# Kernel tuning notes

Hardware: AMD Instinct MI355X
Metric: run time of the kernel (lower is better)

Reference implementation:

```python
import jax, jax.numpy as jnp
import numpy as np
import math

D_MODEL, N_LEVELS, N_HEADS, N_POINTS = 256, 4, 8, 4
D_HEAD = D_MODEL // N_HEADS
SPATIAL = np.array([[128, 128], [64, 64], [32, 32], [16, 16]], dtype=np.int32)  # (H_l, W_l)
LEN_IN = int((SPATIAL[:, 0] * SPATIAL[:, 1]).sum())  # 21760
N_BATCH, LEN_Q = 8, 1000


def _offset_bias():
    # torch _reset_parameters grid_init
    thetas = np.arange(N_HEADS, dtype=np.float32) * (2.0 * math.pi / N_HEADS)
    grid = np.stack([np.cos(thetas), np.sin(thetas)], -1)
    grid = grid / np.abs(grid).max(-1, keepdims=True)
    grid = np.tile(grid.reshape(N_HEADS, 1, 1, 2), (1, N_LEVELS, N_POINTS, 1))
    for i in range(N_POINTS):
        grid[:, :, i, :] *= i + 1
    return jnp.asarray(grid.reshape(-1), dtype=jnp.float32)


def setup_inputs() -> dict:
    key = jax.random.key(0)
    ks = jax.random.split(key, 8)
    s = 1.0 / math.sqrt(D_MODEL)
    return {
        "query": jax.random.normal(ks[0], (N_BATCH, LEN_Q, D_MODEL), jnp.float32),
        "reference_points": jax.random.uniform(ks[1], (N_BATCH, LEN_Q, N_LEVELS, 2), jnp.float32),
        "input_flatten": jax.random.normal(ks[2], (N_BATCH, LEN_IN, D_MODEL), jnp.float32),
        "input_spatial_shapes": jnp.asarray(SPATIAL),
        "input_level_start_index": jnp.asarray(np.concatenate([[0], np.cumsum(SPATIAL[:, 0] * SPATIAL[:, 1])[:-1]]).astype(np.int32)),
        # params (W stored as (in, out); y = x @ W + b)
        "W_off": jax.random.normal(ks[3], (D_MODEL, N_HEADS * N_LEVELS * N_POINTS * 2), jnp.float32) * 0.01,
        "b_off": _offset_bias(),
        "W_attn": jax.random.normal(ks[4], (D_MODEL, N_HEADS * N_LEVELS * N_POINTS), jnp.float32) * 0.02,
        "b_attn": jnp.zeros((N_HEADS * N_LEVELS * N_POINTS,), jnp.float32),
        "W_val": jax.random.normal(ks[5], (D_MODEL, D_MODEL), jnp.float32) * s,
        "b_val": jnp.zeros((D_MODEL,), jnp.float32),
        "W_out": jax.random.normal(ks[6], (D_MODEL, D_MODEL), jnp.float32) * s,
        "b_out": jnp.zeros((D_MODEL,), jnp.float32),
    }


def _bilinear_sample(v, x, y, H, W):
    # v: (N, nH, H*W, dH); x, y: (N, nH, Lq, nP) in pixel coords (grid_sample align_corners=False, zeros padding)
    Nb, nH, Lq, nP = x.shape
    x0 = jnp.floor(x); y0 = jnp.floor(y)
    wx1 = x - x0; wy1 = y - y0
    x0i = x0.astype(jnp.int32); y0i = y0.astype(jnp.int32)
    out = jnp.zeros((Nb, nH, Lq, nP, v.shape[-1]), v.dtype)
    for dy, wy in ((0, 1.0 - wy1), (1, wy1)):
        for dx, wx in ((0, 1.0 - wx1), (1, wx1)):
            ix = x0i + dx; iy = y0i + dy
            valid = (ix >= 0) & (ix < W) & (iy >= 0) & (iy < H)
            idx = (jnp.clip(iy, 0, H - 1) * W + jnp.clip(ix, 0, W - 1)).reshape(Nb, nH, Lq * nP, 1)
            g = jnp.take_along_axis(v, idx, axis=2).reshape(Nb, nH, Lq, nP, -1)
            out = out + g * (wy * wx * valid.astype(v.dtype))[..., None]
    return out


def reference(query, reference_points, input_flatten, input_spatial_shapes, input_level_start_index,
              W_off, b_off, W_attn, b_attn, W_val, b_val, W_out, b_out):
    shapes = np.asarray(input_spatial_shapes)          # static metadata
    starts = np.asarray(input_level_start_index)
    Nb, Lq, _ = query.shape

    value = input_flatten @ W_val + b_val              # (N, Lin, C)
    value = value.reshape(Nb, -1, N_HEADS, D_HEAD).transpose(0, 2, 1, 3)  # (N, nH, Lin, dH)

    offsets = (query @ W_off + b_off).reshape(Nb, Lq, N_HEADS, N_LEVELS, N_POINTS, 2)
    attn = jax.nn.softmax((query @ W_attn + b_attn).reshape(Nb, Lq, N_HEADS, N_LEVELS * N_POINTS), axis=-1)
    attn = attn.reshape(Nb, Lq, N_HEADS, N_LEVELS, N_POINTS)

    # normalizer is (W_l, H_l) per level; locations in [0,1]
    normalizer = jnp.asarray(np.stack([shapes[:, 1], shapes[:, 0]], -1), jnp.float32)
    loc = reference_points[:, :, None, :, None, :] + offsets / normalizer[None, None, None, :, None, :]

    out = jnp.zeros((Nb, N_HEADS, Lq, D_HEAD), value.dtype)
    for l in range(N_LEVELS):
        H, W = int(shapes[l, 0]), int(shapes[l, 1])
        s = int(starts[l])
        v_l = value[:, :, s:s + H * W]                             # (N, nH, HW, dH)
        loc_l = loc[:, :, :, l].transpose(0, 2, 1, 3, 4)           # (N, nH, Lq, nP, 2)
        x = loc_l[..., 0] * W - 0.5
        y = loc_l[..., 1] * H - 0.5
        sampled = _bilinear_sample(v_l, x, y, H, W)                # (N, nH, Lq, nP, dH)
        a_l = attn[:, :, :, l].transpose(0, 2, 1, 3)               # (N, nH, Lq, nP)
        out = out + jnp.einsum('nhqpd,nhqp->nhqd', sampled, a_l)

    out = out.transpose(0, 2, 1, 3).reshape(Nb, Lq, D_MODEL)
    return out @ W_out + b_out
```

## Files before the change

### kernel.cpp

```cpp
#include <hip/hip_runtime.h>
#include <hip/hip_bf16.h>

#define D_MODEL 256
#define N_HEADS 8
#define D_HEAD 32
#define N_LEVELS 4
#define N_POINTS 4
#define LEN_IN 21760
#define N_BATCH 8
#define LEN_Q 1000

typedef __attribute__((ext_vector_type(8))) short short8;
typedef __attribute__((ext_vector_type(4))) float f32x4;
typedef __attribute__((ext_vector_type(4))) unsigned int u32x4;

typedef const __attribute__((address_space(1))) void* gp1;
typedef __attribute__((address_space(3))) void* lp3;

__device__ __forceinline__ unsigned short f2bf(float f) {
    unsigned int u = __float_as_uint(f);
    u += 0x7FFFu + ((u >> 16) & 1u);
    return (unsigned short)(u >> 16);
}
__device__ __forceinline__ float bf2f(unsigned short s) {
    return __uint_as_float(((unsigned int)s) << 16);
}
__device__ __forceinline__ unsigned int cvtpk(float lo, float hi) {
    unsigned int r;
    asm("v_cvt_pk_bf16_f32 %0, %1, %2" : "=v"(r) : "v"(lo), "v"(hi));
    return r;
}

__global__ __launch_bounds__(256) void prep_kernel(
    const float* __restrict__ Wv, const float* __restrict__ Wo,
    const float* __restrict__ Wa, const float* __restrict__ Wu,
    const float* __restrict__ boff, const float* __restrict__ battn,
    unsigned short* __restrict__ WtVp, unsigned short* __restrict__ WtC,
    unsigned short* __restrict__ WtO, float* __restrict__ bcat)
{
    int idx = blockIdx.x * 256 + threadIdx.x;
    if (idx < 65536) {
        int j = idx & 7, lane = (idx >> 3) & 63, nf = (idx >> 9) & 15, ks = idx >> 13;
        int col = nf * 16 + (lane & 15);
        int k = ks * 32 + (lane >> 4) * 8 + j;
        WtVp[idx] = f2bf(Wv[k * 256 + col]);
    } else if (idx < 65536 + 98304) {
        int j = idx - 65536;
        int n = j >> 8, k = j & 255;
        float s = (n < 256) ? Wo[k * 256 + n] : Wa[k * 128 + (n - 256)];
        WtC[j] = f2bf(s);
    } else if (idx < 65536 + 98304 + 65536) {
        int j = idx - (65536 + 98304);
        int n = j >> 8, k = j & 255;
        WtO[j] = f2bf(Wu[k * 256 + n]);
    } else if (idx < 65536 + 98304 + 65536 + 384) {
        int j = idx - (65536 + 98304 + 65536);
        bcat[j] = (j < 256) ? boff[j] : battn[j - 256];
    }
}

__global__ __launch_bounds__(256) void gemm_value(
    const float* __restrict__ A,
    const unsigned short* __restrict__ Bp,
    const float* __restrict__ bias,
    unsigned short* __restrict__ C)
{
    __shared__ __align__(16) float lds[2][4096];

    const int tid = threadIdx.x;
    const int wave = tid >> 6, lane = tid & 63;
    const int lhi = lane >> 4, llo = lane & 15;
    const int mBase = blockIdx.x * 64;

    const int srow = tid >> 4;
    const int scg = (tid & 15) ^ (srow & 15);
    const char* Ab = (const char*)(A + (size_t)mBase * 256);

#define STG(bi, kt) { \
    const char* s_ = Ab + (size_t)(kt) * 256 + (size_t)srow * 1024 + scg * 16; \
    char* d_ = (char*)&lds[bi][0] + tid * 16; \
    __builtin_amdgcn_global_load_lds((gp1)(const void*)(s_),         (lp3)(d_),         16, 0, 0); \
    __builtin_amdgcn_global_load_lds((gp1)(const void*)(s_ + 16384), (lp3)(d_ + 4096),  16, 0, 0); \
    __builtin_amdgcn_global_load_lds((gp1)(const void*)(s_ + 32768), (lp3)(d_ + 8192),  16, 0, 0); \
    __builtin_amdgcn_global_load_lds((gp1)(const void*)(s_ + 49152), (lp3)(d_ + 12288), 16, 0, 0); }

    f32x4 acc[4][4];
#pragma unroll
    for (int mf = 0; mf < 4; ++mf)
#pragma unroll
        for (int n = 0; n < 4; ++n)
            acc[mf][n] = (f32x4){0.f, 0.f, 0.f, 0.f};

    STG(0, 0);

#pragma unroll
    for (int kt = 0; kt < 4; ++kt) {
        const int cur = kt & 1;

        short8 b[2][4];
#pragma unroll
        for (int ksi = 0; ksi < 2; ++ksi)
#pragma unroll
            for (int n = 0; n < 4; ++n)
                b[ksi][n] = *reinterpret_cast<const short8*>(
                    Bp + ((size_t)((kt * 2 + ksi) * 16 + wave * 4 + n) * 64 + lane) * 8);

        if (kt < 3) STG(cur ^ 1, kt + 1);

        __builtin_amdgcn_sched_barrier(0);
        if (kt < 3) asm volatile("s_waitcnt vmcnt(12)" ::: "memory");
        else        asm volatile("s_waitcnt vmcnt(8)" ::: "memory");
        __builtin_amdgcn_sched_barrier(0);
        __builtin_amdgcn_s_barrier();
        __builtin_amdgcn_sched_barrier(0);

#pragma unroll
        for (int mf = 0; mf < 4; ++mf) {
            const int row = mf * 16 + llo;
            const char* rbase = (const char*)&lds[cur][0] + row * 256;
#pragma unroll
            for (int ksi = 0; ksi < 2; ++ksi) {
                const int cg0 = ksi * 8 + lhi * 2;
                f32x4 flo = *reinterpret_cast<const f32x4*>(rbase + ((cg0 ^ llo) << 4));
                f32x4 fhi = *reinterpret_cast<const f32x4*>(rbase + (((cg0 + 1) ^ llo) << 4));
                u32x4 pk;
                pk[0] = cvtpk(flo[0], flo[1]);
                pk[1] = cvtpk(flo[2], flo[3]);
                pk[2] = cvtpk(fhi[0], fhi[1]);
                pk[3] = cvtpk(fhi[2], fhi[3]);
                short8 af = __builtin_bit_cast(short8, pk);
#pragma unroll
                for (int n = 0; n < 4; ++n)
                    acc[mf][n] = __builtin_amdgcn_mfma_f32_16x16x32_bf16(
                        af, b[ksi][n], acc[mf][n], 0, 0, 0);
            }
        }

        __builtin_amdgcn_sched_barrier(0);
        __builtin_amdgcn_s_barrier();
        __builtin_amdgcn_sched_barrier(0);
    }
#undef STG

    float bb[4];
#pragma unroll
    for (int n = 0; n < 4; ++n) bb[n] = bias[wave * 64 + n * 16 + llo];
#pragma unroll
    for (int mf = 0; mf < 4; ++mf) {
        const int row0 = mBase + mf * 16 + lhi * 4;
#pragma unroll
        for (int n = 0; n < 4; ++n) {
            const int col = wave * 64 + n * 16 + llo;
            unsigned int u01 = cvtpk(acc[mf][n][0] + bb[n], acc[mf][n][1] + bb[n]);
            unsigned int u23 = cvtpk(acc[mf][n][2] + bb[n], acc[mf][n][3] + bb[n]);
            C[(size_t)(row0 + 0) * 256 + col] = (unsigned short)(u01 & 0xFFFFu);
            C[(size_t)(row0 + 1) * 256 + col] = (unsigned short)(u01 >> 16);
            C[(size_t)(row0 + 2) * 256 + col] = (unsigned short)(u23 & 0xFFFFu);
            C[(size_t)(row0 + 3) * 256 + col] = (unsigned short)(u23 >> 16);
        }
    }
}

template<int NF, bool ABF16, bool OBF16>
__global__ __launch_bounds__(256) void gemm_k256(
    const void* __restrict__ Av, const unsigned short* __restrict__ Wt,
    const float* __restrict__ bias, void* __restrict__ Cv)
{
    const int wave = threadIdx.x >> 6;
    const int lane = threadIdx.x & 63;
    const int lhi = lane >> 4, llo = lane & 15;
    const int mBase = blockIdx.x * 16;
    const int colBase = wave * (NF * 16);
    const int N = NF * 64;

    f32x4 acc[NF];
#pragma unroll
    for (int n = 0; n < NF; ++n)
        acc[n] = (f32x4){0.f, 0.f, 0.f, 0.f};

#pragma unroll
    for (int ks = 0; ks < 8; ++ks) {
        const int kk = ks * 32 + lhi * 8;
        short8 a;
        if (ABF16) {
            a = *reinterpret_cast<const short8*>(
                (const unsigned short*)Av + (size_t)(mBase + llo) * 256 + kk);
        } else {
            const float* ap = (const float*)Av + (size_t)(mBase + llo) * 256 + kk;
            f32x4 f0 = *reinterpret_cast<const f32x4*>(ap);
            f32x4 f1 = *reinterpret_cast<const f32x4*>(ap + 4);
            u32x4 pk;
            pk[0] = cvtpk(f0[0], f0[1]);
            pk[1] = cvtpk(f0[2], f0[3]);
            pk[2] = cvtpk(f1[0], f1[1]);
            pk[3] = cvtpk(f1[2], f1[3]);
            a = __builtin_bit_cast(short8, pk);
        }
        short8 b[NF];
#pragma unroll
        for (int n = 0; n < NF; ++n) {
            const unsigned short* bp =
                Wt + (size_t)(colBase + n * 16 + llo) * 256 + kk;
            b[n] = *reinterpret_cast<const short8*>(bp);
        }
#pragma unroll
        for (int n = 0; n < NF; ++n)
            acc[n] = __builtin_amdgcn_mfma_f32_16x16x32_bf16(
                a, b[n], acc[n], 0, 0, 0);
    }

    const int row0 = mBase + lhi * 4;
#pragma unroll
    for (int n = 0; n < NF; ++n) {
        const int col = colBase + n * 16 + llo;
        const float bb = bias[col];
#pragma unroll
        for (int r = 0; r < 4; ++r) {
            float v = acc[n][r] + bb;
            size_t idx = (size_t)(row0 + r) * N + col;
            if (OBF16) ((unsigned short*)Cv)[idx] = f2bf(v);
            else       ((float*)Cv)[idx] = v;
        }
    }
}

__global__ __launch_bounds__(512) void ms_sample_kernel(
    const unsigned short* __restrict__ value,
    const float* __restrict__ proj,
    const float* __restrict__ refp,
    unsigned short* __restrict__ out_h)
{
    const int bid = blockIdx.x;
    const int b = bid & 7;
    const int q = bid >> 3;
    const int bq = b * LEN_Q + q;

    const int h = threadIdx.x >> 6;
    const int lane = threadIdx.x & 63;
    const int task = lane >> 2;
    const int l = task >> 2;
    const int qd = lane & 3;

    const float* prow = proj + (size_t)bq * 384;

    const int Wl = 128 >> l;
    const int st = (65536 - (65536 >> (l << 1))) / 3;

    const float2 dxy = *reinterpret_cast<const float2*>(prow + h * 32 + 2 * task);
    const float2 rxy = *reinterpret_cast<const float2*>(refp + ((size_t)bq * 4 + l) * 2);

    const float Wlf = (float)Wl;
    const float x = rxy.x * Wlf + dxy.x - 0.5f;
    const float y = rxy.y * Wlf + dxy.y - 0.5f;
    const float x0f = floorf(x), y0f = floorf(y);
    const int x0 = (int)x0f, y0 = (int)y0f;
    const float wx1 = x - x0f, wy1 = y - y0f;
    const float wx0 = 1.f - wx1, wy0 = 1.f - wy1;

    const int x0c = min(max(x0, 0), Wl - 1);
    const int x1c = min(max(x0 + 1, 0), Wl - 1);
    const int y0c = min(max(y0, 0), Wl - 1);
    const int y1c = min(max(y0 + 1, 0), Wl - 1);
    const float fx0 = (x0 >= 0 && x0 < Wl) ? 1.f : 0.f;
    const float fx1 = (x0 + 1 >= 0 && x0 + 1 < Wl) ? 1.f : 0.f;
    const float fy0 = (y0 >= 0 && y0 < Wl) ? 1.f : 0.f;
    const float fy1 = (y0 + 1 >= 0 && y0 + 1 < Wl) ? 1.f : 0.f;

    const int rr0 = st + y0c * Wl, rr1 = st + y1c * Wl;
    const int r00 = rr0 + x0c, r01 = rr0 + x1c;
    const int r10 = rr1 + x0c, r11 = rr1 + x1c;

    const char* vb = (const char*)value + (size_t)b * LEN_IN * 512
                   + h * 64 + qd * 16;
    u32x4 v0 = *reinterpret_cast<const u32x4*>(vb + (size_t)r00 * 512);
    u32x4 v1 = *reinterpret_cast<const u32x4*>(vb + (size_t)r01 * 512);
    u32x4 v2 = *reinterpret_cast<const u32x4*>(vb + (size_t)r10 * 512);
    u32x4 v3 = *reinterpret_cast<const u32x4*>(vb + (size_t)r11 * 512);

    float lg = prow[256 + h * 16 + (lane & 15)];
    float mx = lg;
    mx = fmaxf(mx, __shfl_xor(mx, 1, 16));
    mx = fmaxf(mx, __shfl_xor(mx, 2, 16));
    mx = fmaxf(mx, __shfl_xor(mx, 4, 16));
    mx = fmaxf(mx, __shfl_xor(mx, 8, 16));
    float e = __expf(lg - mx);
    float den = e;
    den += __shfl_xor(den, 1, 16);
    den += __shfl_xor(den, 2, 16);
    den += __shfl_xor(den, 4, 16);
    den += __shfl_xor(den, 8, 16);
    const float wsm = e / den;
    const float ws = __shfl(wsm, task, 16);

    float wgt[4];
    wgt[0] = ws * wy0 * wx0 * fy0 * fx0;
    wgt[1] = ws * wy0 * wx1 * fy0 * fx1;
    wgt[2] = ws * wy1 * wx0 * fy1 * fx0;
    wgt[3] = ws * wy1 * wx1 * fy1 * fx1;

    float acc[8];
#pragma unroll
    for (int j = 0; j < 8; ++j) acc[j] = 0.f;
#pragma unroll
    for (int n = 0; n < 4; ++n) {
        const u32x4 v = (n == 0) ? v0 : (n == 1) ? v1 : (n == 2) ? v2 : v3;
        const float wn = wgt[n];
#pragma unroll
        for (int j = 0; j < 4; ++j) {
            const unsigned int u = v[j];
            acc[2 * j]     += wn * bf2f((unsigned short)(u & 0xFFFFu));
            acc[2 * j + 1] += wn * bf2f((unsigned short)(u >> 16));
        }
    }

#pragma unroll
    for (int j = 0; j < 8; ++j) {
        acc[j] += __shfl_xor(acc[j], 4, 64);
        acc[j] += __shfl_xor(acc[j], 8, 64);
        acc[j] += __shfl_xor(acc[j], 16, 64);
        acc[j] += __shfl_xor(acc[j], 32, 64);
    }

    if (task == 0) {
        u32x4 o;
#pragma unroll
        for (int j = 0; j < 4; ++j)
            o[j] = (unsigned int)f2bf(acc[2 * j]) |
                   ((unsigned int)f2bf(acc[2 * j + 1]) << 16);
        *reinterpret_cast<u32x4*>(
            out_h + (size_t)bq * 256 + h * 32 + qd * 8) = o;
    }
}

extern "C" void kernel_launch(void* const* d_in, const int* in_sizes, int n_in,
                              void* d_out, int out_size, void* d_ws, size_t ws_size,
                              hipStream_t stream)
{
    const float* query  = (const float*)d_in[0];
    const float* refp   = (const float*)d_in[1];
    const float* inpf   = (const float*)d_in[2];
    const float* W_off  = (const float*)d_in[5];
    const float* b_off  = (const float*)d_in[6];
    const float* W_attn = (const float*)d_in[7];
    const float* b_attn = (const float*)d_in[8];
    const float* W_val  = (const float*)d_in[9];
    const float* b_val  = (const float*)d_in[10];
    const float* W_out  = (const float*)d_in[11];
    const float* b_out  = (const float*)d_in[12];

    char* ws = (char*)d_ws;
    unsigned short* value = (unsigned short*)(ws);
    float*          proj  = (float*)(ws + 89128960);
    unsigned short* out_h = (unsigned short*)(ws + 89128960 + 12288000);
    unsigned short* WtVp  = (unsigned short*)(ws + 109608960);
    unsigned short* WtC   = (unsigned short*)(ws + 109740032);
    unsigned short* WtO   = (unsigned short*)(ws + 109936640);
    float*          bcat  = (float*)(ws + 110067712);

    prep_kernel<<<898, 256, 0, stream>>>(W_val, W_off, W_attn, W_out,
                                         b_off, b_attn, WtVp, WtC, WtO, bcat);

    gemm_value<<<(N_BATCH * LEN_IN) / 64, 256, 0, stream>>>(
        inpf, WtVp, b_val, value);

    gemm_k256<6, false, false><<<(N_BATCH * LEN_Q) / 16, 256, 0, stream>>>(
        query, WtC, bcat, (void*)proj);

    ms_sample_kernel<<<N_BATCH * LEN_Q, 512, 0, stream>>>(
        value, proj, refp, out_h);

    gemm_k256<4, true, false><<<(N_BATCH * LEN_Q) / 16, 256, 0, stream>>>(
        out_h, WtO, b_out, d_out);
}
```

Baseline: 128.5 us.

## Retile value GEMM to 128-row blocks with 8 waves and 32-wide K steps

The value projection GEMM now uses 512-thread blocks covering 128 rows, arranged as a 2x4 wave grid. It stages K in 32-float slices across 8 iterations instead of 64-float slices across 4, keeping the same LDS footprint. Each B fragment load is shared by twice as many rows per block, and the per-step wait count drops. The trade is more barriers per block, half as many blocks, and a new swizzle pattern for LDS reads.

```diff
diff --git a/kernel.cpp b/kernel.cpp
--- a/kernel.cpp
+++ b/kernel.cpp
@@ -59,7 +59,7 @@
     }
 }
 
-__global__ __launch_bounds__(256) void gemm_value(
+__global__ __launch_bounds__(512) void gemm_value(
     const float* __restrict__ A,
     const unsigned short* __restrict__ Bp,
     const float* __restrict__ bias,
@@ -69,20 +69,20 @@
 
     const int tid = threadIdx.x;
     const int wave = tid >> 6, lane = tid & 63;
+    const int wr = wave >> 2, wc = wave & 3;
     const int lhi = lane >> 4, llo = lane & 15;
-    const int mBase = blockIdx.x * 64;
-
-    const int srow = tid >> 4;
-    const int scg = (tid & 15) ^ (srow & 15);
+    const int mBase = blockIdx.x * 128;
+
+    const int srow = tid >> 3;
+    const int scg = (tid & 7) ^ (srow & 7);
     const char* Ab = (const char*)(A + (size_t)mBase * 256);
+    const size_t src0 = (size_t)srow * 1024 + (size_t)scg * 16;
 
 #define STG(bi, kt) { \
-    const char* s_ = Ab + (size_t)(kt) * 256 + (size_t)srow * 1024 + scg * 16; \
+    const char* s_ = Ab + (size_t)(kt) * 128 + src0; \
     char* d_ = (char*)&lds[bi][0] + tid * 16; \
-    __builtin_amdgcn_global_load_lds((gp1)(const void*)(s_),         (lp3)(d_),         16, 0, 0); \
-    __builtin_amdgcn_global_load_lds((gp1)(const void*)(s_ + 16384), (lp3)(d_ + 4096),  16, 0, 0); \
-    __builtin_amdgcn_global_load_lds((gp1)(const void*)(s_ + 32768), (lp3)(d_ + 8192),  16, 0, 0); \
-    __builtin_amdgcn_global_load_lds((gp1)(const void*)(s_ + 49152), (lp3)(d_ + 12288), 16, 0, 0); }
+    __builtin_amdgcn_global_load_lds((gp1)(const void*)(s_),         (lp3)(d_),        16, 0, 0); \
+    __builtin_amdgcn_global_load_lds((gp1)(const void*)(s_ + 65536), (lp3)(d_ + 8192), 16, 0, 0); }
 
     f32x4 acc[4][4];
 #pragma unroll
@@ -94,63 +94,58 @@
     STG(0, 0);
 
 #pragma unroll
-    for (int kt = 0; kt < 4; ++kt) {
+    for (int kt = 0; kt < 8; ++kt) {
         const int cur = kt & 1;
 
-        short8 b[2][4];
-#pragma unroll
-        for (int ksi = 0; ksi < 2; ++ksi)
+        short8 b[4];
+#pragma unroll
+        for (int n = 0; n < 4; ++n)
+            b[n] = *reinterpret_cast<const short8*>(
+                Bp + ((size_t)(kt * 16 + wc * 4 + n) * 64 + lane) * 8);
+
+        if (kt < 7) STG(cur ^ 1, kt + 1);
+
+        __builtin_amdgcn_sched_barrier(0);
+        if (kt < 7) asm volatile("s_waitcnt vmcnt(6)" ::: "memory");
+        else        asm volatile("s_waitcnt vmcnt(4)" ::: "memory");
+        __builtin_amdgcn_sched_barrier(0);
+        __builtin_amdgcn_s_barrier();
+        __builtin_amdgcn_sched_barrier(0);
+
+#pragma unroll
+        for (int mf = 0; mf < 4; ++mf) {
+            const int row = wr * 64 + mf * 16 + llo;
+            const char* rbase = (const char*)&lds[cur][0] + row * 128;
+            const int sw = row & 7;
+            f32x4 flo = *reinterpret_cast<const f32x4*>(rbase + (((lhi * 2) ^ sw) << 4));
+            f32x4 fhi = *reinterpret_cast<const f32x4*>(rbase + (((lhi * 2 + 1) ^ sw) << 4));
+            u32x4 pk;
+            pk[0] = cvtpk(flo[0], flo[1]);
+            pk[1] = cvtpk(flo[2], flo[3]);
+            pk[2] = cvtpk(fhi[0], fhi[1]);
+            pk[3] = cvtpk(fhi[2], fhi[3]);
+            short8 af = __builtin_bit_cast(short8, pk);
 #pragma unroll
             for (int n = 0; n < 4; ++n)
-                b[ksi][n] = *reinterpret_cast<const short8*>(
-                    Bp + ((size_t)((kt * 2 + ksi) * 16 + wave * 4 + n) * 64 + lane) * 8);
-
-        if (kt < 3) STG(cur ^ 1, kt + 1);
-
-        __builtin_amdgcn_sched_barrier(0);
-        if (kt < 3) asm volatile("s_waitcnt vmcnt(12)" ::: "memory");
-        else        asm volatile("s_waitcnt vmcnt(8)" ::: "memory");
+                acc[mf][n] = __builtin_amdgcn_mfma_f32_16x16x32_bf16(
+                    af, b[n], acc[mf][n], 0, 0, 0);
+        }
+
         __builtin_amdgcn_sched_barrier(0);
         __builtin_amdgcn_s_barrier();
         __builtin_amdgcn_sched_barrier(0);
-
-#pragma unroll
-        for (int mf = 0; mf < 4; ++mf) {
-            const int row = mf * 16 + llo;
-            const char* rbase = (const char*)&lds[cur][0] + row * 256;
-#pragma unroll
-            for (int ksi = 0; ksi < 2; ++ksi) {
-                const int cg0 = ksi * 8 + lhi * 2;
-                f32x4 flo = *reinterpret_cast<const f32x4*>(rbase + ((cg0 ^ llo) << 4));
-                f32x4 fhi = *reinterpret_cast<const f32x4*>(rbase + (((cg0 + 1) ^ llo) << 4));
-                u32x4 pk;
-                pk[0] = cvtpk(flo[0], flo[1]);
-                pk[1] = cvtpk(flo[2], flo[3]);
-                pk[2] = cvtpk(fhi[0], fhi[1]);
-                pk[3] = cvtpk(fhi[2], fhi[3]);
-                short8 af = __builtin_bit_cast(short8, pk);
-#pragma unroll
-                for (int n = 0; n < 4; ++n)
-                    acc[mf][n] = __builtin_amdgcn_mfma_f32_16x16x32_bf16(
-                        af, b[ksi][n], acc[mf][n], 0, 0, 0);
-            }
-        }
-
-        __builtin_amdgcn_sched_barrier(0);
-        __builtin_amdgcn_s_barrier();
-        __builtin_amdgcn_sched_barrier(0);
     }
 #undef STG
 
     float bb[4];
 #pragma unroll
-    for (int n = 0; n < 4; ++n) bb[n] = bias[wave * 64 + n * 16 + llo];
+    for (int n = 0; n < 4; ++n) bb[n] = bias[wc * 64 + n * 16 + llo];
 #pragma unroll
     for (int mf = 0; mf < 4; ++mf) {
-        const int row0 = mBase + mf * 16 + lhi * 4;
+        const int row0 = mBase + wr * 64 + mf * 16 + lhi * 4;
 #pragma unroll
         for (int n = 0; n < 4; ++n) {
-            const int col = wave * 64 + n * 16 + llo;
+            const int col = wc * 64 + n * 16 + llo;
             unsigned int u01 = cvtpk(acc[mf][n][0] + bb[n], acc[mf][n][1] + bb[n]);
             unsigned int u23 = cvtpk(acc[mf][n][2] + bb[n], acc[mf][n][3] + bb[n]);
             C[(size_t)(row0 + 0) * 256 + col] = (unsigned short)(u01 & 0xFFFFu);
@@ -360,7 +355,7 @@
     prep_kernel<<<898, 256, 0, stream>>>(W_val, W_off, W_attn, W_out,
                                          b_off, b_attn, WtVp, WtC, WtO, bcat);
 
-    gemm_value<<<(N_BATCH * LEN_IN) / 64, 256, 0, stream>>>(
+    gemm_value<<<(N_BATCH * LEN_IN) / 128, 512, 0, stream>>>(
         inpf, WtVp, b_val, value);
 
     gemm_k256<6, false, false><<<(N_BATCH * LEN_Q) / 16, 256, 0, stream>>>(
```

Result: no change. 130.3 us (+1.5%).

## Process four row tiles per block in value GEMM with continuous prefetch pipeline

Applied to the files above, without the earlier changes.

The value projection GEMM now has each block handle 256 rows as four consecutive 64-row tiles. The global-to-LDS double-buffer pipeline runs across tile boundaries, so the next tile's first K-slice is prefetched while the current tile finishes. Each tile's output is written when it completes. The grid shrinks from 2720 to 680 blocks, which cuts launch and prologue overhead but reduces parallelism to fewer blocks per CU and keeps the B fragments reloaded each step.

```diff
diff --git a/kernel.cpp b/kernel.cpp
--- a/kernel.cpp
+++ b/kernel.cpp
@@ -70,14 +70,15 @@
     const int tid = threadIdx.x;
     const int wave = tid >> 6, lane = tid & 63;
     const int lhi = lane >> 4, llo = lane & 15;
-    const int mBase = blockIdx.x * 64;
+    const size_t rowBlk = (size_t)blockIdx.x * 256;
 
     const int srow = tid >> 4;
     const int scg = (tid & 15) ^ (srow & 15);
-    const char* Ab = (const char*)(A + (size_t)mBase * 256);
-
-#define STG(bi, kt) { \
-    const char* s_ = Ab + (size_t)(kt) * 256 + (size_t)srow * 1024 + scg * 16; \
+    const char* Ab = (const char*)(A + rowBlk * 256);
+    const size_t src0 = (size_t)srow * 1024 + (size_t)scg * 16;
+
+#define STG(bi, tile, kt) { \
+    const char* s_ = Ab + (size_t)(tile) * 65536 + (size_t)(kt) * 256 + src0; \
     char* d_ = (char*)&lds[bi][0] + tid * 16; \
     __builtin_amdgcn_global_load_lds((gp1)(const void*)(s_),         (lp3)(d_),         16, 0, 0); \
     __builtin_amdgcn_global_load_lds((gp1)(const void*)(s_ + 16384), (lp3)(d_ + 4096),  16, 0, 0); \
@@ -91,11 +92,15 @@
         for (int n = 0; n < 4; ++n)
             acc[mf][n] = (f32x4){0.f, 0.f, 0.f, 0.f};
 
-    STG(0, 0);
-
-#pragma unroll
-    for (int kt = 0; kt < 4; ++kt) {
-        const int cur = kt & 1;
+    float bb[4];
+#pragma unroll
+    for (int n = 0; n < 4; ++n) bb[n] = bias[wave * 64 + n * 16 + llo];
+
+    STG(0, 0, 0);
+
+#pragma unroll
+    for (int tau = 0; tau < 16; ++tau) {
+        const int tile = tau >> 2, kt = tau & 3, cur = tau & 1;
 
         short8 b[2][4];
 #pragma unroll
@@ -105,11 +110,14 @@
                 b[ksi][n] = *reinterpret_cast<const short8*>(
                     Bp + ((size_t)((kt * 2 + ksi) * 16 + wave * 4 + n) * 64 + lane) * 8);
 
-        if (kt < 3) STG(cur ^ 1, kt + 1);
-
-        __builtin_amdgcn_sched_barrier(0);
-        if (kt < 3) asm volatile("s_waitcnt vmcnt(12)" ::: "memory");
-        else        asm volatile("s_waitcnt vmcnt(8)" ::: "memory");
+        if (tau < 15) {
+            const int nt = tau + 1;
+            STG(nt & 1, nt >> 2, nt & 3);
+        }
+
+        __builtin_amdgcn_sched_barrier(0);
+        if (tau < 15) asm volatile("s_waitcnt vmcnt(12)" ::: "memory");
+        else          asm volatile("s_waitcnt vmcnt(8)" ::: "memory");
         __builtin_amdgcn_sched_barrier(0);
         __builtin_amdgcn_s_barrier();
         __builtin_amdgcn_sched_barrier(0);
@@ -139,26 +147,26 @@
         __builtin_amdgcn_sched_barrier(0);
         __builtin_amdgcn_s_barrier();
         __builtin_amdgcn_sched_barrier(0);
+
+        if (kt == 3) {
+#pragma unroll
+            for (int mf = 0; mf < 4; ++mf) {
+                const int row0 = (int)rowBlk + tile * 64 + mf * 16 + lhi * 4;
+#pragma unroll
+                for (int n = 0; n < 4; ++n) {
+                    const int col = wave * 64 + n * 16 + llo;
+                    unsigned int u01 = cvtpk(acc[mf][n][0] + bb[n], acc[mf][n][1] + bb[n]);
+                    unsigned int u23 = cvtpk(acc[mf][n][2] + bb[n], acc[mf][n][3] + bb[n]);
+                    C[(size_t)(row0 + 0) * 256 + col] = (unsigned short)(u01 & 0xFFFFu);
+                    C[(size_t)(row0 + 1) * 256 + col] = (unsigned short)(u01 >> 16);
+                    C[(size_t)(row0 + 2) * 256 + col] = (unsigned short)(u23 & 0xFFFFu);
+                    C[(size_t)(row0 + 3) * 256 + col] = (unsigned short)(u23 >> 16);
+                    acc[mf][n] = (f32x4){0.f, 0.f, 0.f, 0.f};
+                }
+            }
+        }
     }
 #undef STG
-
-    float bb[4];
-#pragma unroll
-    for (int n = 0; n < 4; ++n) bb[n] = bias[wave * 64 + n * 16 + llo];
-#pragma unroll
-    for (int mf = 0; mf < 4; ++mf) {
-        const int row0 = mBase + mf * 16 + lhi * 4;
-#pragma unroll
-        for (int n = 0; n < 4; ++n) {
-            const int col = wave * 64 + n * 16 + llo;
-            unsigned int u01 = cvtpk(acc[mf][n][0] + bb[n], acc[mf][n][1] + bb[n]);
-            unsigned int u23 = cvtpk(acc[mf][n][2] + bb[n], acc[mf][n][3] + bb[n]);
-            C[(size_t)(row0 + 0) * 256 + col] = (unsigned short)(u01 & 0xFFFFu);
-            C[(size_t)(row0 + 1) * 256 + col] = (unsigned short)(u01 >> 16);
-            C[(size_t)(row0 + 2) * 256 + col] = (unsigned short)(u23 & 0xFFFFu);
-            C[(size_t)(row0 + 3) * 256 + col] = (unsigned short)(u23 >> 16);
-        }
-    }
 }
 
 template<int NF, bool ABF16, bool OBF16>
@@ -360,8 +368,7 @@
     prep_kernel<<<898, 256, 0, stream>>>(W_val, W_off, W_attn, W_out,
                                          b_off, b_attn, WtVp, WtC, WtO, bcat);
 
-    gemm_value<<<(N_BATCH * LEN_IN) / 64, 256, 0, stream>>>(
-        inpf, WtVp, b_val, value);
+    gemm_value<<<680, 256, 0, stream>>>(inpf, WtVp, b_val, value);
 
     gemm_k256<6, false, false><<<(N_BATCH * LEN_Q) / 16, 256, 0, stream>>>(
         query, WtC, bcat, (void*)proj);
```

After: 139.8 us. 8.9% more time.
